# Kernel tuning notes

Hardware: AMD Instinct MI355X
Metric: run time of the kernel (lower is better)

The kernel has to match this reference:

```python
import jax, jax.numpy as jnp
import numpy as np
from jax import lax

SIGMA = 1
KSIZE = SIGMA * 4 + 1  # 5-tap, odd -> torch 'same' == lax 'SAME'


def _gauss1d():
    half = (KSIZE - 1) * 0.5
    x = np.linspace(-half, half, KSIZE)
    pdf = np.exp(-0.5 * (x / SIGMA) ** 2)
    return jnp.asarray(pdf / pdf.sum(), dtype=jnp.float32)


def _blur(x):
    # separable depthwise 3D gaussian blur: three sequential 1D convs (D, H, W)
    k = _gauss1d().astype(x.dtype)
    C = x.shape[1]
    dn = lax.conv_dimension_numbers(x.shape, (C, 1, KSIZE, 1, 1), ('NCDHW', 'OIDHW', 'NCDHW'))
    for ax in range(3):
        kshape = [1, 1, 1]
        kshape[ax] = KSIZE
        w = jnp.broadcast_to(k.reshape(kshape)[None, None], (C, 1, *kshape))
        x = lax.conv_general_dilated(x, w, (1, 1, 1), 'SAME',
                                     dimension_numbers=dn, feature_group_count=C)
    return x


def setup_inputs() -> dict:
    key = jax.random.key(0)
    kA, kB, kM = jax.random.split(key, 3)
    shape = (2, 1, 160, 192, 224)
    return {
        'image_A': jax.random.normal(kA, shape, dtype=jnp.float32),
        'image_B': jax.random.normal(kB, shape, dtype=jnp.float32),
        'mask_A': jax.random.uniform(kM, shape, dtype=jnp.float32),
    }


def reference(image_A, image_B, mask_A):
    I, J = image_A, image_B
    bI = _blur(I)
    bJ = _blur(J)
    cross = _blur(I * J) - bI * bJ
    varI = jax.nn.relu(_blur(I * I) - bI ** 2) + 1e-05
    varJ = jax.nn.relu(_blur(J * J) - bJ ** 2) + 1e-05
    lncc = 1.0 - cross / jnp.sqrt(varI * varJ)
    return jnp.sum(lncc * mask_A) / (jnp.sum(mask_A) + 1e-08)
```

## Files before the change

kernel.cpp:

```cpp
#include <hip/hip_runtime.h>


#define NB 2
#define DD 160
#define HH 192
#define WW 224
#define SH 224
#define SD (224*192)
#define SN (224*192*160)

#define TW 32
#define TH 16
#define ROWS (TH+4)
#define DCHUNK 20
#define NCHUNK (DD/DCHUNK)

#define K0 0.05448868f
#define K1 0.24420134f
#define K2 0.40261995f

__global__ __launch_bounds__(640) void lncc_main(
    const float* __restrict__ A, const float* __restrict__ B,
    const float* __restrict__ M, double* __restrict__ acc)
{
    __shared__ float2 sIJ[2][ROWS][36];
    __shared__ float4 wbA[2][ROWS][32];
    __shared__ float  wbC[2][ROWS][32];
    __shared__ float  redL[10], redM[10];

    const int wt = blockIdx.x;
    const int ht = blockIdx.y;
    const int zz = blockIdx.z;
    const int n  = zz >> 3;
    const int dc = zz & 7;
    const int w0 = wt * TW, h0 = ht * TH, d0 = dc * DCHUNK;

    const float* __restrict__ Ai = A + (size_t)n * SN;
    const float* __restrict__ Bi = B + (size_t)n * SN;
    const float* __restrict__ Mi = M + (size_t)n * SN;

    const int tid = threadIdx.x;
    const int r   = tid >> 5;
    const int c   = tid & 31;

    const int gh  = h0 + r - 2;
    const bool hv = (unsigned)gh < (unsigned)HH;
    const int ghc = hv ? gh : 0;
    const int hwm = ghc * SH + (w0 + c);
    const int gwl = w0 + c - 2, gwr = w0 + c + 2;
    const bool lv = hv && (c < 2)   && (gwl >= 0);
    const bool rv = hv && (c >= 30) && (gwr < WW);
    const bool anyh = lv || rv;
    const int hwh = ghc * SH + (lv ? gwl : (rv ? gwr : 0));
    const int mbase = (h0 + r) * SH + (w0 + c);

    float pI0=0.f,pI1=0.f,pI2=0.f,pI3=0.f;
    float pJ0=0.f,pJ1=0.f,pJ2=0.f,pJ3=0.f;
    float pC0=0.f,pC1=0.f,pC2=0.f,pC3=0.f;
    float pS0=0.f,pS1=0.f,pS2=0.f,pS3=0.f;
    float pT0=0.f,pT1=0.f,pT2=0.f,pT3=0.f;
    float accL = 0.f, accM = 0.f;

    float nI = 0.f, nJ = 0.f, nHI = 0.f, nHJ = 0.f;
    {
        const int dd = d0 - 2;
        if (dd >= 0) {
            const int dof = dd * SD;
            if (hv)   { nI  = Ai[dof + hwm]; nJ  = Bi[dof + hwm]; }
            if (anyh) { nHI = Ai[dof + hwh]; nHJ = Bi[dof + hwh]; }
        }
    }

    const int NIT = DCHUNK + 6;
    for (int k = 0; k < NIT; ++k) {
        const int pw = k & 1;
        const int px = pw ^ 1;

        if (k < DCHUNK + 4) {
            sIJ[pw][r][c + 2] = make_float2(nI, nJ);
            if (c < 2)        sIJ[pw][r][c]     = make_float2(nHI, nHJ);
            else if (c >= 30) sIJ[pw][r][c + 4] = make_float2(nHI, nHJ);
        }

        nI = nJ = nHI = nHJ = 0.f;
        {
            const int dd = d0 - 1 + k;
            if ((k + 1 < DCHUNK + 4) && (dd >= 0) && (dd < DD)) {
                const int dof = dd * SD;
                if (hv)   { nI  = Ai[dof + hwm]; nJ  = Bi[dof + hwm]; }
                if (anyh) { nHI = Ai[dof + hwh]; nHJ = Bi[dof + hwh]; }
            }
        }
        const int  dout = d0 - 6 + k;
        const bool outv = (k >= 6) && (r < TH);
        float mval = 0.f;
        if (outv) mval = Mi[dout * SD + mbase];

        if (k >= 1 && k <= DCHUNK + 4) {
            const float2 v0 = sIJ[px][r][c];
            const float2 v1 = sIJ[px][r][c + 1];
            const float2 v2 = sIJ[px][r][c + 2];
            const float2 v3 = sIJ[px][r][c + 3];
            const float2 v4 = sIJ[px][r][c + 4];
            const float bi  = K0*(v0.x+v4.x) + K1*(v1.x+v3.x) + K2*v2.x;
            const float bj  = K0*(v0.y+v4.y) + K1*(v1.y+v3.y) + K2*v2.y;
            const float bij = K0*(v0.x*v0.y+v4.x*v4.y) + K1*(v1.x*v1.y+v3.x*v3.y) + K2*v2.x*v2.y;
            const float bii = K0*(v0.x*v0.x+v4.x*v4.x) + K1*(v1.x*v1.x+v3.x*v3.x) + K2*v2.x*v2.x;
            const float bjj = K0*(v0.y*v0.y+v4.y*v4.y) + K1*(v1.y*v1.y+v3.y*v3.y) + K2*v2.y*v2.y;
            wbA[px][r][c] = make_float4(bi, bii, bj, bjj);
            wbC[px][r][c] = bij;
        }

        if (k >= 2 && r < TH) {
            const float4 a0 = wbA[pw][r][c];
            const float4 a1 = wbA[pw][r + 1][c];
            const float4 a2 = wbA[pw][r + 2][c];
            const float4 a3 = wbA[pw][r + 3][c];
            const float4 a4 = wbA[pw][r + 4][c];
            const float c0 = wbC[pw][r][c];
            const float c1 = wbC[pw][r + 1][c];
            const float c2 = wbC[pw][r + 2][c];
            const float c3 = wbC[pw][r + 3][c];
            const float c4 = wbC[pw][r + 4][c];
            const float hI  = K0*(a0.x+a4.x) + K1*(a1.x+a3.x) + K2*a2.x;
            const float hII = K0*(a0.y+a4.y) + K1*(a1.y+a3.y) + K2*a2.y;
            const float hJ  = K0*(a0.z+a4.z) + K1*(a1.z+a3.z) + K2*a2.z;
            const float hJJ = K0*(a0.w+a4.w) + K1*(a1.w+a3.w) + K2*a2.w;
            const float hIJ = K0*(c0+c4)     + K1*(c1+c3)     + K2*c2;

            if (outv) {
                const float bI  = K0*(pI0+hI)  + K1*(pI1+pI3) + K2*pI2;
                const float bJ  = K0*(pJ0+hJ)  + K1*(pJ1+pJ3) + K2*pJ2;
                const float bIJ = K0*(pC0+hIJ) + K1*(pC1+pC3) + K2*pC2;
                const float bII = K0*(pS0+hII) + K1*(pS1+pS3) + K2*pS2;
                const float bJJ = K0*(pT0+hJJ) + K1*(pT1+pT3) + K2*pT2;
                const float cross = bIJ - bI * bJ;
                const float vI = fmaxf(bII - bI * bI, 0.f) + 1e-5f;
                const float vJ = fmaxf(bJJ - bJ * bJ, 0.f) + 1e-5f;
                const float lncc = 1.0f - cross * rsqrtf(vI * vJ);
                accL += lncc * mval;
                accM += mval;
            }

            pI0=pI1; pI1=pI2; pI2=pI3; pI3=hI;
            pJ0=pJ1; pJ1=pJ2; pJ2=pJ3; pJ3=hJ;
            pC0=pC1; pC1=pC2; pC2=pC3; pC3=hIJ;
            pS0=pS1; pS1=pS2; pS2=pS3; pS3=hII;
            pT0=pT1; pT1=pT2; pT2=pT3; pT3=hJJ;
        }

        __syncthreads();
    }

#pragma unroll
    for (int off = 32; off > 0; off >>= 1) {
        accL += __shfl_down(accL, off, 64);
        accM += __shfl_down(accM, off, 64);
    }
    const int wave = tid >> 6;
    if ((tid & 63) == 0) { redL[wave] = accL; redM[wave] = accM; }
    __syncthreads();
    if (tid == 0) {
        float sL = 0.f, sM = 0.f;
#pragma unroll
        for (int kk = 0; kk < 10; ++kk) { sL += redL[kk]; sM += redM[kk]; }
        atomicAdd(&acc[0], (double)sL);
        atomicAdd(&acc[1], (double)sM);
    }
}

__global__ void lncc_final(const double* __restrict__ acc, float* __restrict__ out)
{
    out[0] = (float)(acc[0] / (acc[1] + 1e-8));
}

extern "C" void kernel_launch(void* const* d_in, const int* in_sizes, int n_in,
                              void* d_out, int out_size, void* d_ws, size_t ws_size,
                              hipStream_t stream)
{
    const float* A = (const float*)d_in[0];
    const float* B = (const float*)d_in[1];
    const float* M = (const float*)d_in[2];
    double* acc = (double*)d_ws;

    hipMemsetAsync(d_ws, 0, 2 * sizeof(double), stream);

    dim3 grid(WW / TW, HH / TH, NB * NCHUNK);
    dim3 block(640);
    hipLaunchKernelGGL(lncc_main, grid, block, 0, stream, A, B, M, acc);
    hipLaunchKernelGGL(lncc_final, dim3(1), dim3(1), 0, stream, acc, (float*)d_out);
}
```

Measured before the change: 235.3 us.

## Process two W columns per thread with float2 loads and halve block size

Each thread now handles two adjacent W outputs, so the block shrinks from 640 to 320 threads and global loads become float2 while LDS accesses become float4. The W-blur reuses the six loaded neighbours for two outputs, cutting LDS reads and redundant products per output. The H-blur and D-ring registers are doubled into pairs. This trades higher register pressure and lower thread-level parallelism for fewer memory instructions and less shared-memory traffic per output.

Measured after the change: 376.1 us. +59.9%, slower.

```diff
diff --git a/kernel.cpp b/kernel.cpp
--- a/kernel.cpp
+++ b/kernel.cpp
@@ -11,7 +11,8 @@
 
 #define TW 32
 #define TH 16
-#define ROWS (TH+4)
+#define ROWS 20
+#define CP 16
 #define DCHUNK 20
 #define NCHUNK (DD/DCHUNK)
 
@@ -19,14 +20,21 @@
 #define K1 0.24420134f
 #define K2 0.40261995f
 
-__global__ __launch_bounds__(640) void lncc_main(
+struct F2 { float x, y; };
+__device__ __forceinline__ F2 mkf2(float a, float b) { F2 r; r.x = a; r.y = b; return r; }
+
+#define DOT5(p0,p1,p2,p3,p4) mkf2( \
+    K0*((p0).x+(p4).x) + K1*((p1).x+(p3).x) + K2*(p2).x, \
+    K0*((p0).y+(p4).y) + K1*((p1).y+(p3).y) + K2*(p2).y)
+
+__global__ __launch_bounds__(320) void lncc_main(
     const float* __restrict__ A, const float* __restrict__ B,
     const float* __restrict__ M, double* __restrict__ acc)
 {
     __shared__ float2 sIJ[2][ROWS][36];
-    __shared__ float4 wbA[2][ROWS][32];
-    __shared__ float  wbC[2][ROWS][32];
-    __shared__ float  redL[10], redM[10];
+    __shared__ float4 wbP[2][ROWS][2*CP + 1];
+    __shared__ float2 wbC2[2][ROWS][CP + 1];
+    __shared__ float  redL[5], redM[5];
 
     const int wt = blockIdx.x;
     const int ht = blockIdx.y;
@@ -40,34 +48,33 @@
     const float* __restrict__ Mi = M + (size_t)n * SN;
 
     const int tid = threadIdx.x;
-    const int r   = tid >> 5;
-    const int c   = tid & 31;
+    const int r   = tid >> 4;
+    const int c   = tid & 15;
 
     const int gh  = h0 + r - 2;
     const bool hv = (unsigned)gh < (unsigned)HH;
     const int ghc = hv ? gh : 0;
-    const int hwm = ghc * SH + (w0 + c);
-    const int gwl = w0 + c - 2, gwr = w0 + c + 2;
-    const bool lv = hv && (c < 2)   && (gwl >= 0);
-    const bool rv = hv && (c >= 30) && (gwr < WW);
-    const bool anyh = lv || rv;
-    const int hwh = ghc * SH + (lv ? gwl : (rv ? gwr : 0));
-    const int mbase = (h0 + r) * SH + (w0 + c);
-
-    float pI0=0.f,pI1=0.f,pI2=0.f,pI3=0.f;
-    float pJ0=0.f,pJ1=0.f,pJ2=0.f,pJ3=0.f;
-    float pC0=0.f,pC1=0.f,pC2=0.f,pC3=0.f;
-    float pS0=0.f,pS1=0.f,pS2=0.f,pS3=0.f;
-    float pT0=0.f,pT1=0.f,pT2=0.f,pT3=0.f;
-    float accL = 0.f, accM = 0.f;
-
-    float nI = 0.f, nJ = 0.f, nHI = 0.f, nHJ = 0.f;
+    const int hwm = ghc * SH + (w0 + 2 * c);
+    const bool lh = (c == 0)  && (wt > 0);
+    const bool rh = (c == 15) && (wt < 6);
+    const bool anyh = (lh || rh) && hv;
+    const int hwh = ghc * SH + (lh ? (w0 - 2) : (w0 + 32));
+    const int mbase = (h0 + r) * SH + (w0 + 2 * c);
+
+    F2 pI0=mkf2(0,0),pI1=pI0,pI2=pI0,pI3=pI0;
+    F2 pJ0=pI0,pJ1=pI0,pJ2=pI0,pJ3=pI0;
+    F2 pC0=pI0,pC1=pI0,pC2=pI0,pC3=pI0;
+    F2 pS0=pI0,pS1=pI0,pS2=pI0,pS3=pI0;
+    F2 pT0=pI0,pT1=pI0,pT2=pI0,pT3=pI0;
+    F2 accL=pI0, accM=pI0;
+
+    float2 nIa = {0,0}, nJa = {0,0}, nIh = {0,0}, nJh = {0,0};
     {
         const int dd = d0 - 2;
         if (dd >= 0) {
             const int dof = dd * SD;
-            if (hv)   { nI  = Ai[dof + hwm]; nJ  = Bi[dof + hwm]; }
-            if (anyh) { nHI = Ai[dof + hwh]; nHJ = Bi[dof + hwh]; }
+            if (hv)   { nIa = *(const float2*)(Ai + dof + hwm); nJa = *(const float2*)(Bi + dof + hwm); }
+            if (anyh) { nIh = *(const float2*)(Ai + dof + hwh); nJh = *(const float2*)(Bi + dof + hwh); }
         }
     }
 
@@ -77,69 +84,80 @@
         const int px = pw ^ 1;
 
         if (k < DCHUNK + 4) {
-            sIJ[pw][r][c + 2] = make_float2(nI, nJ);
-            if (c < 2)        sIJ[pw][r][c]     = make_float2(nHI, nHJ);
-            else if (c >= 30) sIJ[pw][r][c + 4] = make_float2(nHI, nHJ);
-        }
-
-        nI = nJ = nHI = nHJ = 0.f;
+            *(float4*)&sIJ[pw][r][2 + 2 * c] = make_float4(nIa.x, nJa.x, nIa.y, nJa.y);
+            if (c == 0)       *(float4*)&sIJ[pw][r][0]  = make_float4(nIh.x, nJh.x, nIh.y, nJh.y);
+            else if (c == 15) *(float4*)&sIJ[pw][r][34] = make_float4(nIh.x, nJh.x, nIh.y, nJh.y);
+        }
+
+        nIa = make_float2(0.f, 0.f); nJa = nIa; nIh = nIa; nJh = nIa;
         {
             const int dd = d0 - 1 + k;
             if ((k + 1 < DCHUNK + 4) && (dd >= 0) && (dd < DD)) {
                 const int dof = dd * SD;
-                if (hv)   { nI  = Ai[dof + hwm]; nJ  = Bi[dof + hwm]; }
-                if (anyh) { nHI = Ai[dof + hwh]; nHJ = Bi[dof + hwh]; }
+                if (hv)   { nIa = *(const float2*)(Ai + dof + hwm); nJa = *(const float2*)(Bi + dof + hwm); }
+                if (anyh) { nIh = *(const float2*)(Ai + dof + hwh); nJh = *(const float2*)(Bi + dof + hwh); }
             }
         }
         const int  dout = d0 - 6 + k;
         const bool outv = (k >= 6) && (r < TH);
-        float mval = 0.f;
-        if (outv) mval = Mi[dout * SD + mbase];
+        float2 mv = make_float2(0.f, 0.f);
+        if (outv) mv = *(const float2*)(Mi + dout * SD + mbase);
 
         if (k >= 1 && k <= DCHUNK + 4) {
-            const float2 v0 = sIJ[px][r][c];
-            const float2 v1 = sIJ[px][r][c + 1];
-            const float2 v2 = sIJ[px][r][c + 2];
-            const float2 v3 = sIJ[px][r][c + 3];
-            const float2 v4 = sIJ[px][r][c + 4];
-            const float bi  = K0*(v0.x+v4.x) + K1*(v1.x+v3.x) + K2*v2.x;
-            const float bj  = K0*(v0.y+v4.y) + K1*(v1.y+v3.y) + K2*v2.y;
-            const float bij = K0*(v0.x*v0.y+v4.x*v4.y) + K1*(v1.x*v1.y+v3.x*v3.y) + K2*v2.x*v2.y;
-            const float bii = K0*(v0.x*v0.x+v4.x*v4.x) + K1*(v1.x*v1.x+v3.x*v3.x) + K2*v2.x*v2.x;
-            const float bjj = K0*(v0.y*v0.y+v4.y*v4.y) + K1*(v1.y*v1.y+v3.y*v3.y) + K2*v2.y*v2.y;
-            wbA[px][r][c] = make_float4(bi, bii, bj, bjj);
-            wbC[px][r][c] = bij;
+            const float4* srow = (const float4*)&sIJ[px][r][0];
+            const float4 q0 = srow[c];
+            const float4 q1 = srow[c + 1];
+            const float4 q2 = srow[c + 2];
+            const float i0=q0.x, j0=q0.y, i1=q0.z, j1=q0.w;
+            const float i2=q1.x, j2=q1.y, i3=q1.z, j3=q1.w;
+            const float i4=q2.x, j4=q2.y, i5=q2.z, j5=q2.w;
+            const float p0=i0*j0, p1=i1*j1, p2=i2*j2, p3=i3*j3, p4=i4*j4, p5=i5*j5;
+            const float s0=i0*i0, s1=i1*i1, s2=i2*i2, s3=i3*i3, s4=i4*i4, s5=i5*i5;
+            const float t0=j0*j0, t1=j1*j1, t2=j2*j2, t3=j3*j3, t4=j4*j4, t5=j5*j5;
+            const F2 bi  = mkf2(K0*(i0+i4)+K1*(i1+i3)+K2*i2, K0*(i1+i5)+K1*(i2+i4)+K2*i3);
+            const F2 bj  = mkf2(K0*(j0+j4)+K1*(j1+j3)+K2*j2, K0*(j1+j5)+K1*(j2+j4)+K2*j3);
+            const F2 bij = mkf2(K0*(p0+p4)+K1*(p1+p3)+K2*p2, K0*(p1+p5)+K1*(p2+p4)+K2*p3);
+            const F2 bii = mkf2(K0*(s0+s4)+K1*(s1+s3)+K2*s2, K0*(s1+s5)+K1*(s2+s4)+K2*s3);
+            const F2 bjj = mkf2(K0*(t0+t4)+K1*(t1+t3)+K2*t2, K0*(t1+t5)+K1*(t2+t4)+K2*t3);
+            wbP[px][r][2*c]     = make_float4(bi.x, bi.y, bii.x, bii.y);
+            wbP[px][r][2*c + 1] = make_float4(bj.x, bj.y, bjj.x, bjj.y);
+            wbC2[px][r][c]      = make_float2(bij.x, bij.y);
         }
 
         if (k >= 2 && r < TH) {
-            const float4 a0 = wbA[pw][r][c];
-            const float4 a1 = wbA[pw][r + 1][c];
-            const float4 a2 = wbA[pw][r + 2][c];
-            const float4 a3 = wbA[pw][r + 3][c];
-            const float4 a4 = wbA[pw][r + 4][c];
-            const float c0 = wbC[pw][r][c];
-            const float c1 = wbC[pw][r + 1][c];
-            const float c2 = wbC[pw][r + 2][c];
-            const float c3 = wbC[pw][r + 3][c];
-            const float c4 = wbC[pw][r + 4][c];
-            const float hI  = K0*(a0.x+a4.x) + K1*(a1.x+a3.x) + K2*a2.x;
-            const float hII = K0*(a0.y+a4.y) + K1*(a1.y+a3.y) + K2*a2.y;
-            const float hJ  = K0*(a0.z+a4.z) + K1*(a1.z+a3.z) + K2*a2.z;
-            const float hJJ = K0*(a0.w+a4.w) + K1*(a1.w+a3.w) + K2*a2.w;
-            const float hIJ = K0*(c0+c4)     + K1*(c1+c3)     + K2*c2;
+            F2 hI=mkf2(0,0), hII=hI, hJ=hI, hJJ=hI, hIJ=hI;
+            const float kt[5] = {K0, K1, K2, K1, K0};
+#pragma unroll
+            for (int t = 0; t < 5; ++t) {
+                const float4 u = wbP[pw][r + t][2*c];
+                const float4 v = wbP[pw][r + t][2*c + 1];
+                const float2 w = wbC2[pw][r + t][c];
+                const float kk = kt[t];
+                hI.x  = fmaf(kk, u.x, hI.x);  hI.y  = fmaf(kk, u.y, hI.y);
+                hII.x = fmaf(kk, u.z, hII.x); hII.y = fmaf(kk, u.w, hII.y);
+                hJ.x  = fmaf(kk, v.x, hJ.x);  hJ.y  = fmaf(kk, v.y, hJ.y);
+                hJJ.x = fmaf(kk, v.z, hJJ.x); hJJ.y = fmaf(kk, v.w, hJJ.y);
+                hIJ.x = fmaf(kk, w.x, hIJ.x); hIJ.y = fmaf(kk, w.y, hIJ.y);
+            }
 
             if (outv) {
-                const float bI  = K0*(pI0+hI)  + K1*(pI1+pI3) + K2*pI2;
-                const float bJ  = K0*(pJ0+hJ)  + K1*(pJ1+pJ3) + K2*pJ2;
-                const float bIJ = K0*(pC0+hIJ) + K1*(pC1+pC3) + K2*pC2;
-                const float bII = K0*(pS0+hII) + K1*(pS1+pS3) + K2*pS2;
-                const float bJJ = K0*(pT0+hJJ) + K1*(pT1+pT3) + K2*pT2;
-                const float cross = bIJ - bI * bJ;
-                const float vI = fmaxf(bII - bI * bI, 0.f) + 1e-5f;
-                const float vJ = fmaxf(bJJ - bJ * bJ, 0.f) + 1e-5f;
-                const float lncc = 1.0f - cross * rsqrtf(vI * vJ);
-                accL += lncc * mval;
-                accM += mval;
+                const F2 bI  = DOT5(pI0, pI1, pI2, pI3, hI);
+                const F2 bJ  = DOT5(pJ0, pJ1, pJ2, pJ3, hJ);
+                const F2 bIJ = DOT5(pC0, pC1, pC2, pC3, hIJ);
+                const F2 bII = DOT5(pS0, pS1, pS2, pS3, hII);
+                const F2 bJJ = DOT5(pT0, pT1, pT2, pT3, hJJ);
+                const float cx  = bIJ.x - bI.x * bJ.x;
+                const float cy  = bIJ.y - bI.y * bJ.y;
+                const float vIx = fmaxf(bII.x - bI.x * bI.x, 0.f) + 1e-5f;
+                const float vIy = fmaxf(bII.y - bI.y * bI.y, 0.f) + 1e-5f;
+                const float vJx = fmaxf(bJJ.x - bJ.x * bJ.x, 0.f) + 1e-5f;
+                const float vJy = fmaxf(bJJ.y - bJ.y * bJ.y, 0.f) + 1e-5f;
+                const float lx = 1.0f - cx * rsqrtf(vIx * vJx);
+                const float ly = 1.0f - cy * rsqrtf(vIy * vJy);
+                accL.x = fmaf(lx, mv.x, accL.x);
+                accL.y = fmaf(ly, mv.y, accL.y);
+                accM.x += mv.x;
+                accM.y += mv.y;
             }
 
             pI0=pI1; pI1=pI2; pI2=pI3; pI3=hI;
@@ -152,18 +170,20 @@
         __syncthreads();
     }
 
+    float aL = accL.x + accL.y;
+    float aM = accM.x + accM.y;
 #pragma unroll
     for (int off = 32; off > 0; off >>= 1) {
-        accL += __shfl_down(accL, off, 64);
-        accM += __shfl_down(accM, off, 64);
+        aL += __shfl_down(aL, off, 64);
+        aM += __shfl_down(aM, off, 64);
     }
     const int wave = tid >> 6;
-    if ((tid & 63) == 0) { redL[wave] = accL; redM[wave] = accM; }
+    if ((tid & 63) == 0) { redL[wave] = aL; redM[wave] = aM; }
     __syncthreads();
     if (tid == 0) {
         float sL = 0.f, sM = 0.f;
 #pragma unroll
-        for (int kk = 0; kk < 10; ++kk) { sL += redL[kk]; sM += redM[kk]; }
+        for (int kk = 0; kk < 5; ++kk) { sL += redL[kk]; sM += redM[kk]; }
         atomicAdd(&acc[0], (double)sL);
         atomicAdd(&acc[1], (double)sM);
     }
@@ -186,7 +206,7 @@
     hipMemsetAsync(d_ws, 0, 2 * sizeof(double), stream);
 
     dim3 grid(WW / TW, HH / TH, NB * NCHUNK);
-    dim3 block(640);
+    dim3 block(320);
     hipLaunchKernelGGL(lncc_main, grid, block, 0, stream, A, B, M, acc);
     hipLaunchKernelGGL(lncc_final, dim3(1), dim3(1), 0, stream, acc, (float*)d_out);
 }
```
